# Optimization experiments

Measured on AMD Instinct MI355X. Metric: run time of the kernel, lower is better.

The kernel has to match this reference:

```python
import math
import jax, jax.numpy as jnp
import numpy as np

B, DIN, DOUT = 16384, 512, 512
LATERAL_K = 3
K_WTA = max(1, int(DOUT * 0.25))


def _build_L_mask(dout: int, k: int) -> np.ndarray:
    m = np.zeros((dout, dout), dtype=np.float32)
    for j in range(dout):
        nb = []
        for off in range(1, k + 1):
            if j - off >= 0:
                nb.append(j - off)
            if j + off < dout:
                nb.append(j + off)
        for n in nb[:k]:
            m[j, n] = 1.0
    return m


def _kwta_mask(x):
    # top-k winner-take-all mask along last dim (ties resolved like torch.topk)
    _, idx = jax.lax.top_k(x, K_WTA)
    rows = jnp.arange(x.shape[0])[:, None]
    return jnp.zeros_like(x).at[rows, idx].set(1.0)


def _phi(x, mask):
    return jax.nn.gelu(x, approximate=False) * mask


def _phi_deriv(x, mask):
    cdf = 0.5 * (1.0 + jax.lax.erf(x / math.sqrt(2.0)))
    pdf = jnp.exp(-0.5 * x * x) / math.sqrt(2.0 * math.pi)
    return (cdf + x * pdf) * mask


def _clip_update(d, max_norm):
    n = jnp.linalg.norm(d)  # global norm over the whole tensor, as in torch
    return jnp.where(n > max_norm, d * (max_norm / (n + 1e-8)), d)


def setup_inputs() -> dict:
    key = jax.random.key(0)
    ks = jax.random.split(key, 8)
    k_v = math.sqrt(1.0 / DIN)
    k_w = math.sqrt(1.0 / DOUT)
    return {
        "bottom_up": jax.random.normal(ks[0], (B, DIN), jnp.float32),
        "td_target": jax.random.normal(ks[1], (B, DOUT), jnp.float32) * 0.5,
        "x": jax.random.normal(ks[2], (B, DOUT), jnp.float32) * 0.5,
        "V": jax.random.uniform(ks[3], (DIN, DOUT), jnp.float32, -k_v, k_v),
        "b_in": jnp.full((DOUT,), -5.0, jnp.float32),
        "W_snap": jax.random.uniform(ks[4], (DOUT, DIN), jnp.float32, -k_w, k_w),
        "b_out_snap": jnp.zeros((DIN,), jnp.float32),
        "L": jax.random.uniform(ks[5], (DOUT, DOUT), jnp.float32, -0.1, 0.1),
        "L_mask": jnp.asarray(_build_L_mask(DOUT, LATERAL_K)),
        "step_i": 2,
    }


def reference(bottom_up, td_target, x, V, b_in, W_snap, b_out_snap, L, L_mask, step_i):
    tau, eta_x, lambda_act = 0.5, 0.8, 1e-6
    mask = _kwta_mask(x)
    phi_x = _phi(x, mask)                                     # [B, DOUT]
    prediction = phi_x @ W_snap + b_out_snap                  # [B, DIN]
    error = jax.lax.stop_gradient(bottom_up - prediction)     # detached in torch
    feedback_drive = (error @ W_snap.T) * _phi_deriv(x, mask)
    forward_drive = bottom_up @ V + b_in                      # [B, DOUT]
    recognition_drive = forward_drive - x                     # recognition_weight=1.0
    top_down_drive = 3.0 * (td_target - x)
    lateral_drive = phi_x @ (L * L_mask)
    state_grad = (feedback_drive + recognition_drive + top_down_drive
                  + 0.3 * lateral_drive - lambda_act * jnp.sign(x))
    eta = eta_x / (1.0 + 0.1 * step_i)
    dx = _clip_update(tau * eta * state_grad, 1.0)
    return jnp.clip(x + dx, -5.0, 5.0)
```

## Files before the change

### kernel.cpp

```cpp
#include <hip/hip_runtime.h>
#include <hip/hip_bf16.h>
#include <cstdint>


#define DEV static __device__ __forceinline__

typedef __attribute__((ext_vector_type(8))) short short8;
typedef __attribute__((ext_vector_type(4))) float f32x4;

static constexpr int BATCH = 16384;
static constexpr int D = 512;

DEV unsigned short f2bf(float f) {
  unsigned u = __float_as_uint(f);
  return (unsigned short)((u + 0x7FFFu + ((u >> 16) & 1u)) >> 16);
}
DEV float bf2f(unsigned short h) { return __uint_as_float(((unsigned)h) << 16); }

DEV int wsum(int v)   { for (int o = 32; o; o >>= 1) v += __shfl_xor(v, o, 64); return v; }
DEV float wsumf(float v) { for (int o = 32; o; o >>= 1) v += __shfl_xor(v, o, 64); return v; }

DEV void gload16(const void* g, void* l) {
  __builtin_amdgcn_global_load_lds((const __attribute__((address_space(1))) void*)g,
                                   (__attribute__((address_space(3))) void*)l, 16, 0, 0);
}

DEV void load8(const float* rowp, int lane, float v[8]) {
  const float4* q = (const float4*)rowp;
  float4 a = q[lane * 2], b = q[lane * 2 + 1];
  v[0] = a.x; v[1] = a.y; v[2] = a.z; v[3] = a.w;
  v[4] = b.x; v[5] = b.y; v[6] = b.z; v[7] = b.w;
}

__global__ __launch_bounds__(256) void prep_k(
    const float* __restrict__ W, const float* __restrict__ V,
    const float* __restrict__ L, const float* __restrict__ Lm,
    unsigned short* __restrict__ Wbt, unsigned short* __restrict__ Wb2,
    unsigned short* __restrict__ Vbt, float* __restrict__ Mc,
    float* __restrict__ ssq)
{
  int idx = blockIdx.x * 256 + threadIdx.x;
  int n = idx >> 9, k = idx & 511;
  Wbt[idx] = f2bf(W[k * D + n]);
  Wb2[idx] = f2bf(W[idx]);
  Vbt[idx] = f2bf(V[k * D + n]);
  if (idx < D * 7) {
    int nn = idx / 7, t = idx - nn * 7;
    int j = nn - 3 + t;
    float v = 0.f;
    if (j >= 0 && j < D && j != nn) v = L[j * D + nn] * Lm[j * D + nn];
    Mc[idx] = v;
  }
  if (idx == 0) *ssq = 0.f;
}

__global__ __launch_bounds__(256) void kwta_k(
    const float* __restrict__ x, const float* __restrict__ td,
    const float* __restrict__ bu, const float* __restrict__ b_in,
    const float* __restrict__ Mc,
    unsigned short* __restrict__ phi16, unsigned short* __restrict__ pd16,
    unsigned short* __restrict__ base16, unsigned short* __restrict__ bu16)
{
  __shared__ float phibuf[4][D];
  const int tid = threadIdx.x, lane = tid & 63, wv = tid >> 6;
  const int row = blockIdx.x * 4 + wv;
  const size_t rbase = (size_t)row * D;

  float xv[8];
  load8(x + rbase, lane, xv);
  unsigned key[8];
  #pragma unroll
  for (int s = 0; s < 8; ++s) {
    unsigned u = __float_as_uint(xv[s]);
    key[s] = (u & 0x80000000u) ? ~u : (u | 0x80000000u);
  }
  unsigned T = 0u;
  for (int bit = 31; bit >= 0; --bit) {
    unsigned cand = T | (1u << bit);
    int c = 0;
    #pragma unroll
    for (int s = 0; s < 8; ++s) c += (key[s] >= cand);
    if (wsum(c) >= 128) T = cand;
  }
  int cg = 0;
  #pragma unroll
  for (int s = 0; s < 8; ++s) cg += (key[s] > T);
  const int rneed = 128 - wsum(cg);
  bool eq[8]; int le = 0;
  #pragma unroll
  for (int s = 0; s < 8; ++s) { eq[s] = (key[s] == T); le += eq[s] ? 1 : 0; }
  int pre = le;
  for (int o = 1; o < 64; o <<= 1) { int v = __shfl_up(pre, o, 64); if (lane >= o) pre += v; }
  int run = pre - le;

  float phiv[8], pdv[8];
  float* pb = phibuf[wv];
  #pragma unroll
  for (int s = 0; s < 8; ++s) {
    bool sel = key[s] > T;
    if (eq[s]) { sel = (run < rneed); ++run; }
    float v = xv[s];
    float cdf = 0.5f * (1.0f + erff(v * 0.7071067811865476f));
    float ph = sel ? v * cdf : 0.0f;
    float pd = sel ? (cdf + v * 0.3989422804014327f * __expf(-0.5f * v * v)) : 0.0f;
    phiv[s] = ph; pdv[s] = pd;
    pb[lane * 8 + s] = ph;
  }
  __syncthreads();

  float tdv[8], buv[8];
  load8(td + rbase, lane, tdv);
  load8(bu + rbase, lane, buv);

  short8 o_phi, o_pd, o_base, o_bu;
  #pragma unroll
  for (int s = 0; s < 8; ++s) {
    int n = lane * 8 + s;
    float lat = 0.f;
    #pragma unroll
    for (int t = 0; t < 7; ++t) {
      int j = n - 3 + t;
      int jc = j < 0 ? 0 : (j > D - 1 ? D - 1 : j);
      lat += Mc[n * 7 + t] * pb[jc];
    }
    float v = xv[s];
    float sgn = (v > 0.f) ? 1.f : ((v < 0.f) ? -1.f : 0.f);
    float bs = b_in[n] + 3.f * tdv[s] - 4.f * v + 0.3f * lat - 1e-6f * sgn;
    o_phi[s] = (short)f2bf(phiv[s]);
    o_pd[s]  = (short)f2bf(pdv[s]);
    o_base[s]= (short)f2bf(bs);
    o_bu[s]  = (short)f2bf(buv[s]);
  }
  *(short8*)(phi16 + rbase + lane * 8) = o_phi;
  *(short8*)(pd16  + rbase + lane * 8) = o_pd;
  *(short8*)(base16+ rbase + lane * 8) = o_base;
  *(short8*)(bu16  + rbase + lane * 8) = o_bu;
}

template<int MODE>
__global__ __launch_bounds__(256) void gemm_k(
    const unsigned short* __restrict__ A,
    const unsigned short* __restrict__ Bt,
    const float* __restrict__ f32a,
    const float* __restrict__ f32b,
    const unsigned short* __restrict__ b16a,
    const unsigned short* __restrict__ b16b,
    unsigned short* __restrict__ out16,
    float* __restrict__ outf,
    float* __restrict__ ssq,
    const int* __restrict__ stepi)
{
  constexpr int K = 512;
  __shared__ __align__(16) unsigned short As[128 * 32];
  __shared__ __align__(16) unsigned short Bs[128 * 32];
  const int tid = threadIdx.x;
  const int lane = tid & 63, w = tid >> 6;
  const int m0 = (blockIdx.x >> 2) * 128, n0 = (blockIdx.x & 3) * 128;
  const int qr = (w >> 1) * 64, qc = (w & 1) * 64;
  const int lr = lane & 15, g = lane >> 4;

  f32x4 acc[4][4];
  #pragma unroll
  for (int m = 0; m < 4; ++m)
    #pragma unroll
    for (int n = 0; n < 4; ++n) acc[m][n] = (f32x4){0.f, 0.f, 0.f, 0.f};

  const unsigned short* Abase = A + (size_t)m0 * K;
  const unsigned short* Bbase = Bt + (size_t)n0 * K;

  for (int kt = 0; kt < K; kt += 32) {
    #pragma unroll
    for (int p = 0; p < 2; ++p) {
      int ch = tid + p * 256;
      int row = ch >> 2, kc = (ch & 3) * 8;
      gload16(Abase + (size_t)row * K + kt + kc, As + (size_t)(w * 64 + p * 256) * 8);
      gload16(Bbase + (size_t)row * K + kt + kc, Bs + (size_t)(w * 64 + p * 256) * 8);
    }
    __syncthreads();
    short8 af[4], bfr[4];
    #pragma unroll
    for (int m = 0; m < 4; ++m) af[m]  = *(const short8*)(As + (qr + 16 * m + lr) * 32 + 8 * g);
    #pragma unroll
    for (int n = 0; n < 4; ++n) bfr[n] = *(const short8*)(Bs + (qc + 16 * n + lr) * 32 + 8 * g);
    #pragma unroll
    for (int m = 0; m < 4; ++m)
      #pragma unroll
      for (int n = 0; n < 4; ++n)
        acc[m][n] = __builtin_amdgcn_mfma_f32_16x16x32_bf16(af[m], bfr[n], acc[m][n], 0, 0, 0);
    __syncthreads();
  }

  float tau_eta = 0.f, lssq = 0.f;
  if constexpr (MODE == 3) tau_eta = 0.5f * 0.8f / (1.0f + 0.1f * (float)stepi[0]);
  #pragma unroll
  for (int m = 0; m < 4; ++m) {
    #pragma unroll
    for (int n = 0; n < 4; ++n) {
      #pragma unroll
      for (int r = 0; r < 4; ++r) {
        int row = m0 + qr + 16 * m + 4 * g + r;
        int col = n0 + qc + 16 * n + lr;
        size_t idx = (size_t)row * D + col;
        float v = acc[m][n][r];
        if constexpr (MODE == 1) {
          out16[idx] = f2bf(f32a[idx] - (v + f32b[col]));
        } else if constexpr (MODE == 2) {
          out16[idx] = f2bf(v * bf2f(b16a[idx]));
        } else {
          float dv = tau_eta * (v + bf2f(b16a[idx]) + bf2f(b16b[idx]));
          outf[idx] = dv;
          lssq += dv * dv;
        }
      }
    }
  }
  if constexpr (MODE == 3) {
    lssq = wsumf(lssq);
    if (lane == 0) atomicAdd(ssq, lssq);
  }
}

__global__ __launch_bounds__(256) void final_k(const float* __restrict__ x,
                                               float* __restrict__ d,
                                               const float* __restrict__ ssq)
{
  float nrm = sqrtf(*ssq);
  float s = nrm > 1.0f ? 1.0f / (nrm + 1e-8f) : 1.0f;
  int i = blockIdx.x * 256 + threadIdx.x;
  const float4* xq = (const float4*)x;
  float4* dq = (float4*)d;
  float4 xv = xq[i], dv = dq[i];
  float4 o;
  o.x = fminf(fmaxf(xv.x + s * dv.x, -5.f), 5.f);
  o.y = fminf(fmaxf(xv.y + s * dv.y, -5.f), 5.f);
  o.z = fminf(fmaxf(xv.z + s * dv.z, -5.f), 5.f);
  o.w = fminf(fmaxf(xv.w + s * dv.w, -5.f), 5.f);
  dq[i] = o;
}

extern "C" void kernel_launch(void* const* d_in, const int* in_sizes, int n_in,
                              void* d_out, int out_size, void* d_ws, size_t ws_size,
                              hipStream_t stream) {
  const float* bu    = (const float*)d_in[0];
  const float* td    = (const float*)d_in[1];
  const float* x     = (const float*)d_in[2];
  const float* V     = (const float*)d_in[3];
  const float* b_in  = (const float*)d_in[4];
  const float* W     = (const float*)d_in[5];
  const float* bout  = (const float*)d_in[6];
  const float* L     = (const float*)d_in[7];
  const float* Lm    = (const float*)d_in[8];
  const int*   stepi = (const int*)d_in[9];
  float* dout = (float*)d_out;

  char* p = (char*)d_ws;
  size_t off = 0;
  auto take = [&](size_t bytes) -> void* {
    void* r = (void*)(p + off);
    off += (bytes + 255) & ~(size_t)255;
    return r;
  };
  float* ssq            = (float*)take(4);
  unsigned short* Wbt   = (unsigned short*)take((size_t)D * D * 2);
  unsigned short* Wb2   = (unsigned short*)take((size_t)D * D * 2);
  unsigned short* Vbt   = (unsigned short*)take((size_t)D * D * 2);
  float* Mc             = (float*)take((size_t)D * 7 * 4);
  const size_t bd = (size_t)BATCH * D * 2;
  unsigned short* phi16 = (unsigned short*)take(bd);
  unsigned short* bu16  = (unsigned short*)take(bd);
  unsigned short* pd16  = (unsigned short*)take(bd);
  unsigned short* bse16 = (unsigned short*)take(bd);
  unsigned short* err16 = (unsigned short*)take(bd);
  unsigned short* fb16  = phi16;

  prep_k<<<(D * D) / 256, 256, 0, stream>>>(W, V, L, Lm, Wbt, Wb2, Vbt, Mc, ssq);
  kwta_k<<<BATCH / 4, 256, 0, stream>>>(x, td, bu, b_in, Mc, phi16, pd16, bse16, bu16);
  gemm_k<1><<<(BATCH / 128) * (D / 128), 256, 0, stream>>>(
      phi16, Wbt, bu, bout, nullptr, nullptr, err16, nullptr, nullptr, nullptr);
  gemm_k<2><<<(BATCH / 128) * (D / 128), 256, 0, stream>>>(
      err16, Wb2, nullptr, nullptr, pd16, nullptr, fb16, nullptr, nullptr, nullptr);
  gemm_k<3><<<(BATCH / 128) * (D / 128), 256, 0, stream>>>(
      bu16, Vbt, nullptr, nullptr, fb16, bse16, nullptr, dout, ssq, stepi);
  final_k<<<(BATCH * D / 4) / 256, 256, 0, stream>>>(x, dout, ssq);
}
```

Before: 283.1 us.

## Use ballot-based k-WTA, conflict-free lateral LDS layout, and bf16 bottom-up in GEMM1

The k-WTA threshold search replaces shuffle-reduction wave sums with ballot+popcount, and the tie prefix count uses ballot masks. The phi scratch buffer is stored in a strided layout to avoid LDS bank conflicts, and the lateral band matrix is transposed so each lane loads its coefficients as float4 vectors. The first GEMM epilogue now reads the bf16 copy of bottom_up instead of the fp32 original, which halves that read traffic but adds extra rounding to the error term.

```diff
diff --git a/kernel.cpp b/kernel.cpp
--- a/kernel.cpp
+++ b/kernel.cpp
@@ -17,7 +17,6 @@
 }
 DEV float bf2f(unsigned short h) { return __uint_as_float(((unsigned)h) << 16); }
 
-DEV int wsum(int v)   { for (int o = 32; o; o >>= 1) v += __shfl_xor(v, o, 64); return v; }
 DEV float wsumf(float v) { for (int o = 32; o; o >>= 1) v += __shfl_xor(v, o, 64); return v; }
 
 DEV void gload16(const void* g, void* l) {
@@ -36,7 +35,7 @@
     const float* __restrict__ W, const float* __restrict__ V,
     const float* __restrict__ L, const float* __restrict__ Lm,
     unsigned short* __restrict__ Wbt, unsigned short* __restrict__ Wb2,
-    unsigned short* __restrict__ Vbt, float* __restrict__ Mc,
+    unsigned short* __restrict__ Vbt, float* __restrict__ Mc7,
     float* __restrict__ ssq)
 {
   int idx = blockIdx.x * 256 + threadIdx.x;
@@ -44,12 +43,12 @@
   Wbt[idx] = f2bf(W[k * D + n]);
   Wb2[idx] = f2bf(W[idx]);
   Vbt[idx] = f2bf(V[k * D + n]);
-  if (idx < D * 7) {
-    int nn = idx / 7, t = idx - nn * 7;
+  if (idx < 7 * D) {
+    int t = idx >> 9, nn = idx & 511;
     int j = nn - 3 + t;
     float v = 0.f;
     if (j >= 0 && j < D && j != nn) v = L[j * D + nn] * Lm[j * D + nn];
-    Mc[idx] = v;
+    Mc7[idx] = v;
   }
   if (idx == 0) *ssq = 0.f;
 }
@@ -57,11 +56,11 @@
 __global__ __launch_bounds__(256) void kwta_k(
     const float* __restrict__ x, const float* __restrict__ td,
     const float* __restrict__ bu, const float* __restrict__ b_in,
-    const float* __restrict__ Mc,
+    const float* __restrict__ Mc7,
     unsigned short* __restrict__ phi16, unsigned short* __restrict__ pd16,
     unsigned short* __restrict__ base16, unsigned short* __restrict__ bu16)
 {
-  __shared__ float phibuf[4][D];
+  __shared__ float pbuf[4][D];
   const int tid = threadIdx.x, lane = tid & 63, wv = tid >> 6;
   const int row = blockIdx.x * 4 + wv;
   const size_t rbase = (size_t)row * D;
@@ -79,32 +78,34 @@
     unsigned cand = T | (1u << bit);
     int c = 0;
     #pragma unroll
-    for (int s = 0; s < 8; ++s) c += (key[s] >= cand);
-    if (wsum(c) >= 128) T = cand;
+    for (int s = 0; s < 8; ++s) c += (int)__popcll(__ballot(key[s] >= cand));
+    T = (c >= 128) ? cand : T;
   }
   int cg = 0;
-  #pragma unroll
-  for (int s = 0; s < 8; ++s) cg += (key[s] > T);
-  const int rneed = 128 - wsum(cg);
-  bool eq[8]; int le = 0;
-  #pragma unroll
-  for (int s = 0; s < 8; ++s) { eq[s] = (key[s] == T); le += eq[s] ? 1 : 0; }
-  int pre = le;
-  for (int o = 1; o < 64; o <<= 1) { int v = __shfl_up(pre, o, 64); if (lane >= o) pre += v; }
-  int run = pre - le;
+  unsigned long long em[8];
+  #pragma unroll
+  for (int s = 0; s < 8; ++s) {
+    cg += (int)__popcll(__ballot(key[s] > T));
+    em[s] = __ballot(key[s] == T);
+  }
+  const int rneed = 128 - cg;
+  const unsigned long long lower = (1ull << lane) - 1ull;
+  int run = 0;
+  #pragma unroll
+  for (int s = 0; s < 8; ++s) run += (int)__popcll(em[s] & lower);
 
   float phiv[8], pdv[8];
-  float* pb = phibuf[wv];
+  float* pb = pbuf[wv];
   #pragma unroll
   for (int s = 0; s < 8; ++s) {
     bool sel = key[s] > T;
-    if (eq[s]) { sel = (run < rneed); ++run; }
+    if (key[s] == T) { sel = (run < rneed); ++run; }
     float v = xv[s];
     float cdf = 0.5f * (1.0f + erff(v * 0.7071067811865476f));
     float ph = sel ? v * cdf : 0.0f;
     float pd = sel ? (cdf + v * 0.3989422804014327f * __expf(-0.5f * v * v)) : 0.0f;
     phiv[s] = ph; pdv[s] = pd;
-    pb[lane * 8 + s] = ph;
+    pb[(s << 6) | lane] = ph;
   }
   __syncthreads();
 
@@ -112,20 +113,27 @@
   load8(td + rbase, lane, tdv);
   load8(bu + rbase, lane, buv);
 
+  float lat[8] = {0.f, 0.f, 0.f, 0.f, 0.f, 0.f, 0.f, 0.f};
+  #pragma unroll
+  for (int t = 0; t < 7; ++t) {
+    const float4* mq = (const float4*)(Mc7 + t * D + lane * 8);
+    float4 m0 = mq[0], m1 = mq[1];
+    float mm[8] = {m0.x, m0.y, m0.z, m0.w, m1.x, m1.y, m1.z, m1.w};
+    #pragma unroll
+    for (int s = 0; s < 8; ++s) {
+      int j = lane * 8 + s - 3 + t;
+      int jc = j < 0 ? 0 : (j > D - 1 ? D - 1 : j);
+      lat[s] += mm[s] * pb[((jc & 7) << 6) | (jc >> 3)];
+    }
+  }
+
   short8 o_phi, o_pd, o_base, o_bu;
   #pragma unroll
   for (int s = 0; s < 8; ++s) {
     int n = lane * 8 + s;
-    float lat = 0.f;
-    #pragma unroll
-    for (int t = 0; t < 7; ++t) {
-      int j = n - 3 + t;
-      int jc = j < 0 ? 0 : (j > D - 1 ? D - 1 : j);
-      lat += Mc[n * 7 + t] * pb[jc];
-    }
     float v = xv[s];
     float sgn = (v > 0.f) ? 1.f : ((v < 0.f) ? -1.f : 0.f);
-    float bs = b_in[n] + 3.f * tdv[s] - 4.f * v + 0.3f * lat - 1e-6f * sgn;
+    float bs = b_in[n] + 3.f * tdv[s] - 4.f * v + 0.3f * lat[s] - 1e-6f * sgn;
     o_phi[s] = (short)f2bf(phiv[s]);
     o_pd[s]  = (short)f2bf(pdv[s]);
     o_base[s]= (short)f2bf(bs);
@@ -141,7 +149,6 @@
 __global__ __launch_bounds__(256) void gemm_k(
     const unsigned short* __restrict__ A,
     const unsigned short* __restrict__ Bt,
-    const float* __restrict__ f32a,
     const float* __restrict__ f32b,
     const unsigned short* __restrict__ b16a,
     const unsigned short* __restrict__ b16b,
@@ -203,7 +210,7 @@
         size_t idx = (size_t)row * D + col;
         float v = acc[m][n][r];
         if constexpr (MODE == 1) {
-          out16[idx] = f2bf(f32a[idx] - (v + f32b[col]));
+          out16[idx] = f2bf(bf2f(b16a[idx]) - (v + f32b[col]));
         } else if constexpr (MODE == 2) {
           out16[idx] = f2bf(v * bf2f(b16a[idx]));
         } else {
@@ -264,7 +271,7 @@
   unsigned short* Wbt   = (unsigned short*)take((size_t)D * D * 2);
   unsigned short* Wb2   = (unsigned short*)take((size_t)D * D * 2);
   unsigned short* Vbt   = (unsigned short*)take((size_t)D * D * 2);
-  float* Mc             = (float*)take((size_t)D * 7 * 4);
+  float* Mc7            = (float*)take((size_t)7 * D * 4);
   const size_t bd = (size_t)BATCH * D * 2;
   unsigned short* phi16 = (unsigned short*)take(bd);
   unsigned short* bu16  = (unsigned short*)take(bd);
@@ -273,13 +280,13 @@
   unsigned short* err16 = (unsigned short*)take(bd);
   unsigned short* fb16  = phi16;
 
-  prep_k<<<(D * D) / 256, 256, 0, stream>>>(W, V, L, Lm, Wbt, Wb2, Vbt, Mc, ssq);
-  kwta_k<<<BATCH / 4, 256, 0, stream>>>(x, td, bu, b_in, Mc, phi16, pd16, bse16, bu16);
+  prep_k<<<(D * D) / 256, 256, 0, stream>>>(W, V, L, Lm, Wbt, Wb2, Vbt, Mc7, ssq);
+  kwta_k<<<BATCH / 4, 256, 0, stream>>>(x, td, bu, b_in, Mc7, phi16, pd16, bse16, bu16);
   gemm_k<1><<<(BATCH / 128) * (D / 128), 256, 0, stream>>>(
-      phi16, Wbt, bu, bout, nullptr, nullptr, err16, nullptr, nullptr, nullptr);
+      phi16, Wbt, bout, bu16, nullptr, err16, nullptr, nullptr, nullptr);
   gemm_k<2><<<(BATCH / 128) * (D / 128), 256, 0, stream>>>(
-      err16, Wb2, nullptr, nullptr, pd16, nullptr, fb16, nullptr, nullptr, nullptr);
+      err16, Wb2, nullptr, pd16, nullptr, fb16, nullptr, nullptr, nullptr);
   gemm_k<3><<<(BATCH / 128) * (D / 128), 256, 0, stream>>>(
-      bu16, Vbt, nullptr, nullptr, fb16, bse16, nullptr, dout, ssq, stepi);
+      bu16, Vbt, nullptr, fb16, bse16, nullptr, dout, ssq, stepi);
   final_k<<<(BATCH * D / 4) / 256, 256, 0, stream>>>(x, dout, ssq);
 }
```

Result: faster. 263.4 us (-7.0%).
